# Kernel tuning notes

Hardware: AMD Instinct MI355X
Metric: run time of the kernel (lower is better)

## Reference

```python
import jax, jax.numpy as jnp
import numpy as np

N_RAYS = 65536
N_SAMPLES = 96


def setup_inputs() -> dict:
    key = jax.random.key(0)
    k1, k2, k3 = jax.random.split(key, 3)
    rgb = jax.random.uniform(k1, (N_RAYS, N_SAMPLES, 3), dtype=jnp.float32)
    # SDF values near the surface, small magnitude
    sdf = jax.random.normal(k2, (N_RAYS, N_SAMPLES), dtype=jnp.float32) * 0.1
    # monotonically increasing sample depths along each ray
    z_vals = jnp.sort(
        jax.random.uniform(k3, (N_RAYS, N_SAMPLES), dtype=jnp.float32,
                           minval=0.1, maxval=5.0), axis=-1)
    return {"rgb": rgb, "sdf": sdf, "z_vals": z_vals, "beta": 10}


def reference(rgb, sdf, z_vals, beta):
    # sdf2alpha: alpha = 1 - exp(-beta * sigmoid(-sdf * beta))
    alpha = 1.0 - jnp.exp(-beta * jax.nn.sigmoid(-sdf * beta))  # [N, S]
    # exclusive cumprod of (1 - alpha + 1e-10): transmittance
    trans = jnp.cumprod(
        jnp.concatenate([jnp.ones_like(alpha[:, :1]), 1.0 - alpha + 1e-10],
                        axis=-1), axis=-1)[:, :-1]  # [N, S]
    weights = alpha * trans  # [N, S]
    rendered_rgb = jnp.sum(weights[..., None] * rgb, axis=-2)  # [N, 3]
    rendered_depth = jnp.sum(weights * z_vals, axis=-1)  # [N]
    return (rendered_depth, rendered_rgb, sdf, z_vals)
```

## Files before the change

kernel.cpp:

```cpp
#include <hip/hip_runtime.h>
#include <hip/hip_bf16.h>


#define SDFR_N_SAMPLES 96

__global__ __launch_bounds__(256) void sdf_render_kernel(
    const float*  __restrict__ rgb,
    const float*  __restrict__ sdf,
    const float*  __restrict__ zv,
    const int*    __restrict__ beta_p,
    float* __restrict__ out_depth,
    float* __restrict__ out_rgb,
    float* __restrict__ out_sdf,
    float* __restrict__ out_z,
    int n_rays)
{
    int bi = *beta_p;
    float beta;
    if (bi > 1000000 || bi < -1000000) {
        union { int i; float f; } c; c.i = bi; beta = c.f;
    } else {
        beta = (float)bi;
    }

    const int lane = threadIdx.x & 63;
    const int half = lane >> 5;
    const int l    = lane & 31;
    const int wave = threadIdx.x >> 6;
    const int ray  = (blockIdx.x * 4 + wave) * 2 + half;
    if (ray >= n_rays) return;

    const int base = ray * SDFR_N_SAMPLES + 3 * l;

    const float s0 = sdf[base + 0];
    const float s1 = sdf[base + 1];
    const float s2 = sdf[base + 2];
    const float z0 = zv[base + 0];
    const float z1 = zv[base + 1];
    const float z2 = zv[base + 2];
    const float* rp = rgb + (size_t)base * 3;
    float c[9];
    #pragma unroll
    for (int i = 0; i < 9; ++i) c[i] = rp[i];

    out_sdf[base + 0] = s0;
    out_sdf[base + 1] = s1;
    out_sdf[base + 2] = s2;
    out_z[base + 0]   = z0;
    out_z[base + 1]   = z1;
    out_z[base + 2]   = z2;

    const float e0 = __expf(-beta * __builtin_amdgcn_rcpf(1.0f + __expf(s0 * beta)));
    const float e1 = __expf(-beta * __builtin_amdgcn_rcpf(1.0f + __expf(s1 * beta)));
    const float e2 = __expf(-beta * __builtin_amdgcn_rcpf(1.0f + __expf(s2 * beta)));
    const float a0 = 1.0f - e0, t0 = e0 + 1e-10f;
    const float a1 = 1.0f - e1, t1 = e1 + 1e-10f;
    const float a2 = 1.0f - e2, t2 = e2 + 1e-10f;

    const float m = t0 * t1 * t2;
    float scan = m;
    #pragma unroll
    for (int d = 1; d < 32; d <<= 1) {
        float v = __shfl_up(scan, d, 32);
        if (l >= d) scan *= v;
    }
    float E = __shfl_up(scan, 1, 32);
    if (l == 0) E = 1.0f;

    const float w0 = a0 * E;
    const float w1 = a1 * E * t0;
    const float w2 = a2 * E * t0 * t1;

    float depth = w0 * z0 + w1 * z1 + w2 * z2;
    float r0 = w0 * c[0] + w1 * c[3] + w2 * c[6];
    float r1 = w0 * c[1] + w1 * c[4] + w2 * c[7];
    float r2 = w0 * c[2] + w1 * c[5] + w2 * c[8];

    #pragma unroll
    for (int d = 16; d >= 1; d >>= 1) {
        depth += __shfl_xor(depth, d, 32);
        r0    += __shfl_xor(r0, d, 32);
        r1    += __shfl_xor(r1, d, 32);
        r2    += __shfl_xor(r2, d, 32);
    }

    if (l == 0) {
        out_depth[ray]       = depth;
        out_rgb[ray * 3 + 0] = r0;
        out_rgb[ray * 3 + 1] = r1;
        out_rgb[ray * 3 + 2] = r2;
    }
}

extern "C" void kernel_launch(void* const* d_in, const int* in_sizes, int n_in,
                              void* d_out, int out_size, void* d_ws, size_t ws_size,
                              hipStream_t stream) {
    (void)n_in; (void)d_ws; (void)ws_size; (void)out_size;

    const float* rgb    = (const float*)d_in[0];
    const float* sdf    = (const float*)d_in[1];
    const float* zv     = (const float*)d_in[2];
    const int*   beta_p = (const int*)d_in[3];

    const int n_rays = in_sizes[1] / SDFR_N_SAMPLES;

    float* out_depth = (float*)d_out;
    float* out_rgb   = out_depth + n_rays;
    float* out_sdf   = out_rgb   + (size_t)n_rays * 3;
    float* out_z     = out_sdf   + (size_t)n_rays * SDFR_N_SAMPLES;

    const int rays_per_block = 8;
    const int grid = (n_rays + rays_per_block - 1) / rays_per_block;
    sdf_render_kernel<<<grid, 256, 0, stream>>>(
        rgb, sdf, zv, beta_p, out_depth, out_rgb, out_sdf, out_z, n_rays);
}
```

Measured before the change: 169.8 us.

## Stage ray data through LDS with coalesced float4 loads and stores

Each block now loads its 8 rays' sdf, z and rgb data as fully coalesced float4 accesses, writes the sdf/z passthrough outputs as float4, and stages everything in shared memory. Per-lane compute then reads its three samples from LDS. This replaces the old per-lane strided scalar global loads and stores (12- and 36-byte strides). The cost is a block barrier and about 15 KB of LDS per block, plus redundant clamped loads and stores in the tail threads. A launch-bounds occupancy hint is also added.

```diff
diff --git a/kernel.cpp b/kernel.cpp
--- a/kernel.cpp
+++ b/kernel.cpp
@@ -2,53 +2,84 @@
 #include <hip/hip_bf16.h>
 
 
-#define SDFR_N_SAMPLES 96
+#define SDFR_NS 96
+#define SDFR_RPB 8
 
-__global__ __launch_bounds__(256) void sdf_render_kernel(
-    const float*  __restrict__ rgb,
-    const float*  __restrict__ sdf,
-    const float*  __restrict__ zv,
+__global__ __launch_bounds__(256, 8) void sdf_render_kernel(
+    const float4* __restrict__ rgb4,
+    const float4* __restrict__ sdf4,
+    const float4* __restrict__ z4,
     const int*    __restrict__ beta_p,
-    float* __restrict__ out_depth,
-    float* __restrict__ out_rgb,
-    float* __restrict__ out_sdf,
-    float* __restrict__ out_z,
+    float*  __restrict__ out_depth,
+    float*  __restrict__ out_rgb,
+    float4* __restrict__ out_sdf4,
+    float4* __restrict__ out_z4,
     int n_rays)
 {
+    __shared__ float4 sz_s[384];
+    __shared__ float4 rgb_s[576];
+
+    const int t  = threadIdx.x;
+    const int r0 = blockIdx.x * SDFR_RPB;
+
+    const long base4  = (long)r0 * (SDFR_NS / 4);
+    const long rbase4 = (long)r0 * (SDFR_NS * 3 / 4);
+
+    const int f1 = t;
+    const int f2 = (256 + t > 383) ? 383 : 256 + t;
+    const int g1 = t;
+    const int g2 = 256 + t;
+    const int g3 = (512 + t > 575) ? 575 : 512 + t;
+
+    const float4* p1 = (f1 < 192) ? (sdf4 + base4 + f1)
+                                  : (z4   + base4 + (f1 - 192));
+    const float4* p2 = (f2 < 192) ? (sdf4 + base4 + f2)
+                                  : (z4   + base4 + (f2 - 192));
+
+    const float4 va  = *p1;
+    const float4 vb  = *p2;
+    const float4 vc1 = rgb4[rbase4 + g1];
+    const float4 vc2 = rgb4[rbase4 + g2];
+    const float4 vc3 = rgb4[rbase4 + g3];
+
     int bi = *beta_p;
     float beta;
     if (bi > 1000000 || bi < -1000000) {
-        union { int i; float f; } c; c.i = bi; beta = c.f;
+        union { int i; float f; } u; u.i = bi; beta = u.f;
     } else {
         beta = (float)bi;
     }
 
-    const int lane = threadIdx.x & 63;
-    const int half = lane >> 5;
-    const int l    = lane & 31;
-    const int wave = threadIdx.x >> 6;
-    const int ray  = (blockIdx.x * 4 + wave) * 2 + half;
-    if (ray >= n_rays) return;
+    float4* q1 = (f1 < 192) ? (out_sdf4 + base4 + f1)
+                            : (out_z4   + base4 + (f1 - 192));
+    float4* q2 = (f2 < 192) ? (out_sdf4 + base4 + f2)
+                            : (out_z4   + base4 + (f2 - 192));
+    *q1 = va;
+    *q2 = vb;
 
-    const int base = ray * SDFR_N_SAMPLES + 3 * l;
+    sz_s[f1]  = va;
+    sz_s[f2]  = vb;
+    rgb_s[g1] = vc1;
+    rgb_s[g2] = vc2;
+    rgb_s[g3] = vc3;
 
-    const float s0 = sdf[base + 0];
-    const float s1 = sdf[base + 1];
-    const float s2 = sdf[base + 2];
-    const float z0 = zv[base + 0];
-    const float z1 = zv[base + 1];
-    const float z2 = zv[base + 2];
-    const float* rp = rgb + (size_t)base * 3;
-    float c[9];
-    #pragma unroll
-    for (int i = 0; i < 9; ++i) c[i] = rp[i];
+    __syncthreads();
 
-    out_sdf[base + 0] = s0;
-    out_sdf[base + 1] = s1;
-    out_sdf[base + 2] = s2;
-    out_z[base + 0]   = z0;
-    out_z[base + 1]   = z1;
-    out_z[base + 2]   = z2;
+    const int g   = t >> 5;
+    const int l   = t & 31;
+    const int ray = r0 + g;
+
+    const float* szf  = (const float*)sz_s;
+    const float* rgbf = (const float*)rgb_s;
+
+    const int sb = g * SDFR_NS + 3 * l;
+    const float s0 = szf[sb], s1 = szf[sb + 1], s2 = szf[sb + 2];
+    const float z0 = szf[768 + sb], z1 = szf[768 + sb + 1], z2 = szf[768 + sb + 2];
+
+    const int rb = g * (SDFR_NS * 3) + 9 * l;
+    const float c0 = rgbf[rb + 0], c1 = rgbf[rb + 1], c2 = rgbf[rb + 2];
+    const float c3 = rgbf[rb + 3], c4 = rgbf[rb + 4], c5 = rgbf[rb + 5];
+    const float c6 = rgbf[rb + 6], c7 = rgbf[rb + 7], c8 = rgbf[rb + 8];
 
     const float e0 = __expf(-beta * __builtin_amdgcn_rcpf(1.0f + __expf(s0 * beta)));
     const float e1 = __expf(-beta * __builtin_amdgcn_rcpf(1.0f + __expf(s1 * beta)));
@@ -72,23 +103,23 @@
     const float w2 = a2 * E * t0 * t1;
 
     float depth = w0 * z0 + w1 * z1 + w2 * z2;
-    float r0 = w0 * c[0] + w1 * c[3] + w2 * c[6];
-    float r1 = w0 * c[1] + w1 * c[4] + w2 * c[7];
-    float r2 = w0 * c[2] + w1 * c[5] + w2 * c[8];
+    float r0acc = w0 * c0 + w1 * c3 + w2 * c6;
+    float r1acc = w0 * c1 + w1 * c4 + w2 * c7;
+    float r2acc = w0 * c2 + w1 * c5 + w2 * c8;
 
     #pragma unroll
     for (int d = 16; d >= 1; d >>= 1) {
         depth += __shfl_xor(depth, d, 32);
-        r0    += __shfl_xor(r0, d, 32);
-        r1    += __shfl_xor(r1, d, 32);
-        r2    += __shfl_xor(r2, d, 32);
+        r0acc += __shfl_xor(r0acc, d, 32);
+        r1acc += __shfl_xor(r1acc, d, 32);
+        r2acc += __shfl_xor(r2acc, d, 32);
     }
 
-    if (l == 0) {
+    if (l == 0 && ray < n_rays) {
         out_depth[ray]       = depth;
-        out_rgb[ray * 3 + 0] = r0;
-        out_rgb[ray * 3 + 1] = r1;
-        out_rgb[ray * 3 + 2] = r2;
+        out_rgb[ray * 3 + 0] = r0acc;
+        out_rgb[ray * 3 + 1] = r1acc;
+        out_rgb[ray * 3 + 2] = r2acc;
     }
 }
 
@@ -97,20 +128,20 @@
                               hipStream_t stream) {
     (void)n_in; (void)d_ws; (void)ws_size; (void)out_size;
 
-    const float* rgb    = (const float*)d_in[0];
-    const float* sdf    = (const float*)d_in[1];
-    const float* zv     = (const float*)d_in[2];
-    const int*   beta_p = (const int*)d_in[3];
+    const float4* rgb4   = (const float4*)d_in[0];
+    const float4* sdf4   = (const float4*)d_in[1];
+    const float4* z4     = (const float4*)d_in[2];
+    const int*    beta_p = (const int*)d_in[3];
 
-    const int n_rays = in_sizes[1] / SDFR_N_SAMPLES;
+    const int n_rays = in_sizes[1] / SDFR_NS;
 
     float* out_depth = (float*)d_out;
     float* out_rgb   = out_depth + n_rays;
     float* out_sdf   = out_rgb   + (size_t)n_rays * 3;
-    float* out_z     = out_sdf   + (size_t)n_rays * SDFR_N_SAMPLES;
+    float* out_z     = out_sdf   + (size_t)n_rays * SDFR_NS;
 
-    const int rays_per_block = 8;
-    const int grid = (n_rays + rays_per_block - 1) / rays_per_block;
+    const int grid = (n_rays + SDFR_RPB - 1) / SDFR_RPB;
     sdf_render_kernel<<<grid, 256, 0, stream>>>(
-        rgb, sdf, zv, beta_p, out_depth, out_rgb, out_sdf, out_z, n_rays);
+        rgb4, sdf4, z4, beta_p, out_depth, out_rgb,
+        (float4*)out_sdf, (float4*)out_z, n_rays);
 }
```

After: 169.6 us. No clear change (-0.1%).
